# Performance work log

Hardware: AMD Instinct MI355X
Metric: run time of the kernel (lower is better)

Reference implementation:

```python
import jax, jax.numpy as jnp
import numpy as np

B = 1024          # number of graphs (subjects)
N1_PER = 116      # nodes per graph, branch 1 (AAL atlas)
N2_PER = 200      # nodes per graph, branch 2 (CC200 atlas)
DEG = 16          # sparsified adjacency degree
H = 32            # hidden_dim
NUM_CLASSES = 2


def _make_graph(key, b, n, deg):
    """Block-diagonal sparse adjacency in COO form, deg edges per node within its block."""
    N = b * n
    E = N * deg
    rows = jnp.repeat(jnp.arange(N, dtype=jnp.int32), deg)
    offs = jax.random.randint(jax.random.fold_in(key, 0), (E,), 0, n, dtype=jnp.int32)
    cols = (rows // n) * n + offs
    vals = jax.random.uniform(jax.random.fold_in(key, 1), (E,), dtype=jnp.float32)
    return rows, cols, vals


def setup_inputs() -> dict:
    key = jax.random.key(0)
    ks = jax.random.split(key, 20)
    rows1, cols1, vals1 = _make_graph(ks[0], B, N1_PER, DEG)
    rows2, cols2, vals2 = _make_graph(ks[1], B, N2_PER, DEG)
    x1 = jax.random.normal(ks[2], (B * N1_PER, N1_PER), dtype=jnp.float32)
    x2 = jax.random.normal(ks[3], (B * N2_PER, N2_PER), dtype=jnp.float32)
    s = 0.1
    inp = {
        "rows1": rows1, "cols1": cols1, "vals1": vals1, "x1": x1,
        "rows2": rows2, "cols2": cols2, "vals2": vals2, "x2": x2,
        # GCN branch 116
        "W1a": jax.random.normal(ks[4], (N1_PER, H), dtype=jnp.float32) * s,
        "b1a": jnp.zeros((H,), jnp.float32),
        "W1b": jax.random.normal(ks[5], (H, H), dtype=jnp.float32) * s,
        "b1b": jnp.zeros((H,), jnp.float32),
        # GCN branch 200
        "W2a": jax.random.normal(ks[6], (N2_PER, H), dtype=jnp.float32) * s,
        "b2a": jnp.zeros((H,), jnp.float32),
        "W2b": jax.random.normal(ks[7], (H, H), dtype=jnp.float32) * s,
        "b2b": jnp.zeros((H,), jnp.float32),
        # MLP head (stored as (in, out))
        "fc1_W": jax.random.normal(ks[8], (4 * H, H), dtype=jnp.float32) * s,
        "fc1_b": jnp.zeros((H,), jnp.float32),
        "fc2_W": jax.random.normal(ks[9], (H, H // 2), dtype=jnp.float32) * s,
        "fc2_b": jnp.zeros((H // 2,), jnp.float32),
        "fc3_W": jax.random.normal(ks[10], (H // 2, NUM_CLASSES), dtype=jnp.float32) * s,
        "fc3_b": jnp.zeros((NUM_CLASSES,), jnp.float32),
    }
    return inp


def _gcn(rows, cols, vals, x, W, b):
    # support = X @ W  (dense GEMM), then sparse aggregation A @ support, then bias
    support = x @ W                              # [N, H]
    msg = vals[:, None] * support[cols]          # gather + scale, [E, H]
    agg = jax.ops.segment_sum(msg, rows, num_segments=x.shape[0])  # scatter-add
    return agg + b


def _branch(rows, cols, vals, x, Wa, ba, Wb, bb, n_per):
    h = jax.nn.relu(_gcn(rows, cols, vals, x, Wa, ba))
    h = jax.nn.relu(_gcn(rows, cols, vals, h, Wb, bb))
    h = h.reshape(-1, n_per, h.shape[-1])        # [B, n, H]
    return jnp.concatenate([h.mean(axis=1), h.max(axis=1)], axis=1)  # [B, 2H]


def reference(rows1, cols1, vals1, x1, rows2, cols2, vals2, x2,
              W1a, b1a, W1b, b1b, W2a, b2a, W2b, b2b,
              fc1_W, fc1_b, fc2_W, fc2_b, fc3_W, fc3_b):
    f116 = _branch(rows1, cols1, vals1, x1, W1a, b1a, W1b, b1b, N1_PER)
    f200 = _branch(rows2, cols2, vals2, x2, W2a, b2a, W2b, b2b, N2_PER)
    x = jnp.concatenate([f116, f200], axis=1)    # [B, 4H]
    h = jax.nn.relu(x @ fc1_W + fc1_b)           # dropout is identity at inference
    h = jax.nn.relu(h @ fc2_W + fc2_b)
    logits = h @ fc3_W + fc3_b                   # [B, 2]
    return logits
```

## Files before the change

### kernel.cpp

```cpp
#include <hip/hip_runtime.h>

#define NB 1024
#define N1P 116
#define N2P 200
#define HD 32


template <int ST>
__device__ __forceinline__ void agg_phase(int base, int NPv,
                                          const int* __restrict__ cols,
                                          const float* __restrict__ vals,
                                          const float* __restrict__ sup,
                                          float bias, float* __restrict__ outh,
                                          int tid) {
    const int h = tid & 31;
    for (int n = tid >> 5; n < NPv; n += 8) {
        const int4* c4 = (const int4*)(cols + ((size_t)base + n) * 16);
        const float4* v4 = (const float4*)(vals + ((size_t)base + n) * 16);
        float a = bias;
#pragma unroll
        for (int q = 0; q < 4; ++q) {
            const int4 c = c4[q];
            const float4 v = v4[q];
            a += v.x * sup[(c.x - base) * ST + h];
            a += v.y * sup[(c.y - base) * ST + h];
            a += v.z * sup[(c.z - base) * ST + h];
            a += v.w * sup[(c.w - base) * ST + h];
        }
        outh[n * ST + h] = fmaxf(a, 0.f);
    }
}

template <int NP>
__device__ void branch_graph(int g,
                             const float* __restrict__ X,
                             const int* __restrict__ cols,
                             const float* __restrict__ vals,
                             const float* __restrict__ Wa,
                             const float* __restrict__ ba,
                             const float* __restrict__ Wb,
                             const float* __restrict__ bb,
                             float* __restrict__ feats, int foff,
                             float* sSup, float* sH) {
    constexpr int ST = 33;
    constexpr int KC = 16;
    constexpr int SXS = 20;
    constexpr int NSLOT = NP * 4;
    constexpr int PSL = (NSLOT + 255) / 256;

    const int tid = threadIdx.x;
    const int base = g * NP;
    const float* xg = X + (size_t)base * NP;
    const float bA = ba[tid & 31];
    const float bB = bb[tid & 31];

    float* sX = sSup;

    float acc[32];
#pragma unroll
    for (int c = 0; c < 32; ++c) acc[c] = 0.f;

    const int NC = (NP + KC - 1) / KC;

    float4 cur[PSL], nxt[PSL];

    auto load_chunk = [&](int kc, float4* buf) {
        const int k0 = kc * KC;
        const int kw = (NP - k0) < KC ? (NP - k0) : KC;
        const int pieces = kw >> 2;
#pragma unroll
        for (int q = 0; q < PSL; ++q) {
            const int i = tid + q * 256;
            float4 v = make_float4(0.f, 0.f, 0.f, 0.f);
            if (i < NSLOT) {
                const int row = i >> 2, p = i & 3;
                if (p < pieces)
                    v = *(const float4*)(xg + (size_t)row * NP + k0 + p * 4);
            }
            buf[q] = v;
        }
    };
    auto store_chunk = [&](const float4* buf) {
#pragma unroll
        for (int q = 0; q < PSL; ++q) {
            const int i = tid + q * 256;
            if (i < NSLOT) {
                const int row = i >> 2, p = i & 3;
                *(float4*)&sX[row * SXS + p * 4] = buf[q];
            }
        }
    };

    load_chunk(0, cur);
#pragma unroll 1
    for (int kc = 0; kc < NC; ++kc) {
        __syncthreads();
        store_chunk(cur);
        __syncthreads();
        if (kc + 1 < NC) load_chunk(kc + 1, nxt);
        const int k0 = kc * KC;
        const int kw = (NP - k0) < KC ? (NP - k0) : KC;
        if (tid < NP) {
            const float* xrow = &sX[tid * SXS];
            const float* wb0 = Wa + (size_t)k0 * 32;
#pragma unroll 1
            for (int k4 = 0; k4 < kw; k4 += 4) {
                const float4 x4 = *(const float4*)&xrow[k4];
#pragma unroll
                for (int kk = 0; kk < 4; ++kk) {
                    const float xs = (&x4.x)[kk];
                    const float* w = wb0 + (k4 + kk) * 32;
#pragma unroll
                    for (int c4 = 0; c4 < 8; ++c4) {
                        const float4 wv = *(const float4*)&w[c4 * 4];
                        acc[c4 * 4 + 0] += xs * wv.x;
                        acc[c4 * 4 + 1] += xs * wv.y;
                        acc[c4 * 4 + 2] += xs * wv.z;
                        acc[c4 * 4 + 3] += xs * wv.w;
                    }
                }
            }
        }
#pragma unroll
        for (int q = 0; q < PSL; ++q) cur[q] = nxt[q];
    }
    __syncthreads();

    if (tid < NP) {
#pragma unroll
        for (int c4 = 0; c4 < 8; ++c4) {
            float4 o;
            o.x = acc[c4 * 4 + 0]; o.y = acc[c4 * 4 + 1];
            o.z = acc[c4 * 4 + 2]; o.w = acc[c4 * 4 + 3];
            *(float4*)&sSup[tid * ST + c4 * 4] = o;
        }
    }
    __syncthreads();

    agg_phase<ST>(base, NP, cols, vals, sSup, bA, sH, tid);
    __syncthreads();

    if (tid < NP) {
        float acc2[32];
#pragma unroll
        for (int c = 0; c < 32; ++c) acc2[c] = 0.f;
        const float* xrow = &sH[tid * ST];
#pragma unroll 1
        for (int k4 = 0; k4 < 32; k4 += 4) {
            const float4 x4 = *(const float4*)&xrow[k4];
#pragma unroll
            for (int kk = 0; kk < 4; ++kk) {
                const float xs = (&x4.x)[kk];
                const float* w = Wb + (k4 + kk) * 32;
#pragma unroll
                for (int c4 = 0; c4 < 8; ++c4) {
                    const float4 wv = *(const float4*)&w[c4 * 4];
                    acc2[c4 * 4 + 0] += xs * wv.x;
                    acc2[c4 * 4 + 1] += xs * wv.y;
                    acc2[c4 * 4 + 2] += xs * wv.z;
                    acc2[c4 * 4 + 3] += xs * wv.w;
                }
            }
        }
#pragma unroll
        for (int c4 = 0; c4 < 8; ++c4) {
            float4 o;
            o.x = acc2[c4 * 4 + 0]; o.y = acc2[c4 * 4 + 1];
            o.z = acc2[c4 * 4 + 2]; o.w = acc2[c4 * 4 + 3];
            *(float4*)&sSup[tid * ST + c4 * 4] = o;
        }
    }
    __syncthreads();

    agg_phase<ST>(base, NP, cols, vals, sSup, bB, sH, tid);
    __syncthreads();

    const int h = tid & 31, sl = tid >> 5;
    float sum = 0.f, mx = -1e30f;
    for (int n = sl; n < NP; n += 8) {
        const float v = sH[n * ST + h];
        sum += v;
        mx = fmaxf(mx, v);
    }
    float* sS = sSup;
    float* sM = sSup + 256;
    sS[tid] = sum;
    sM[tid] = mx;
    __syncthreads();
    if (tid < 32) {
#pragma unroll
        for (int q = 1; q < 8; ++q) {
            sum += sS[tid + 32 * q];
            mx = fmaxf(mx, sM[tid + 32 * q]);
        }
        feats[(size_t)g * 128 + foff + tid] = sum * (1.0f / NP);
        feats[(size_t)g * 128 + foff + 32 + tid] = mx;
    }
}

__global__ __launch_bounds__(256, 3) void fused_branches(
        const float* __restrict__ x1, const int* __restrict__ cols1,
        const float* __restrict__ vals1,
        const float* __restrict__ W1a, const float* __restrict__ b1a,
        const float* __restrict__ W1b, const float* __restrict__ b1b,
        const float* __restrict__ x2, const int* __restrict__ cols2,
        const float* __restrict__ vals2,
        const float* __restrict__ W2a, const float* __restrict__ b2a,
        const float* __restrict__ W2b, const float* __restrict__ b2b,
        float* __restrict__ feats) {
    __shared__ float sSup[N2P * 33];
    __shared__ float sH[N2P * 33];
    const int bid = blockIdx.x;
    if (bid < NB) {
        branch_graph<N1P>(bid, x1, cols1, vals1, W1a, b1a, W1b, b1b, feats, 0,
                          sSup, sH);
    } else {
        branch_graph<N2P>(bid - NB, x2, cols2, vals2, W2a, b2a, W2b, b2b, feats,
                          64, sSup, sH);
    }
}

__global__ __launch_bounds__(256) void mlp_head(const float* __restrict__ feats,
                                                const float* __restrict__ W1,
                                                const float* __restrict__ b1,
                                                const float* __restrict__ W2,
                                                const float* __restrict__ b2,
                                                const float* __restrict__ W3,
                                                const float* __restrict__ b3,
                                                float* __restrict__ out) {
    __shared__ float sW1[128 * 32];
    __shared__ float sW2[32 * 16];
    __shared__ float sW3[16 * 2];
    __shared__ float sB1[32], sB2[16], sB3[2];
    __shared__ float sF[8 * 128];
    __shared__ float sH1[8 * 32];
    __shared__ float sH2[8 * 16];

    const int tid = threadIdx.x;
    for (int idx = tid; idx < 128 * 32; idx += 256) sW1[idx] = W1[idx];
    for (int idx = tid; idx < 32 * 16; idx += 256) sW2[idx] = W2[idx];
    if (tid < 32) { sW3[tid] = W3[tid]; sB1[tid] = b1[tid]; }
    if (tid < 16) sB2[tid] = b2[tid];
    if (tid < 2) sB3[tid] = b3[tid];
    const long g0 = (long)blockIdx.x * 8;
    for (int idx = tid; idx < 1024; idx += 256) sF[idx] = feats[g0 * 128 + idx];
    __syncthreads();

    const int g = tid >> 5, h = tid & 31;
    float a1 = sB1[h];
#pragma unroll 4
    for (int k = 0; k < 128; ++k) a1 += sF[g * 128 + k] * sW1[k * 32 + h];
    sH1[g * 32 + h] = fmaxf(a1, 0.f);
    __syncthreads();

    if (h < 16) {
        float a2 = sB2[h];
#pragma unroll
        for (int k = 0; k < 32; ++k) a2 += sH1[g * 32 + k] * sW2[k * 16 + h];
        sH2[g * 16 + h] = fmaxf(a2, 0.f);
    }
    __syncthreads();

    if (h < 2) {
        float a3 = sB3[h];
#pragma unroll
        for (int k = 0; k < 16; ++k) a3 += sH2[g * 16 + k] * sW3[k * 2 + h];
        out[(g0 + g) * 2 + h] = a3;
    }
}

extern "C" void kernel_launch(void* const* d_in, const int* in_sizes, int n_in,
                              void* d_out, int out_size, void* d_ws, size_t ws_size,
                              hipStream_t stream) {
    const int*   cols1 = (const int*)d_in[1];
    const float* vals1 = (const float*)d_in[2];
    const float* x1    = (const float*)d_in[3];
    const int*   cols2 = (const int*)d_in[5];
    const float* vals2 = (const float*)d_in[6];
    const float* x2    = (const float*)d_in[7];
    const float* W1a = (const float*)d_in[8];
    const float* b1a = (const float*)d_in[9];
    const float* W1b = (const float*)d_in[10];
    const float* b1b = (const float*)d_in[11];
    const float* W2a = (const float*)d_in[12];
    const float* b2a = (const float*)d_in[13];
    const float* W2b = (const float*)d_in[14];
    const float* b2b = (const float*)d_in[15];
    const float* fc1_W = (const float*)d_in[16];
    const float* fc1_b = (const float*)d_in[17];
    const float* fc2_W = (const float*)d_in[18];
    const float* fc2_b = (const float*)d_in[19];
    const float* fc3_W = (const float*)d_in[20];
    const float* fc3_b = (const float*)d_in[21];
    float* out = (float*)d_out;

    float* feats = (float*)d_ws;

    fused_branches<<<2 * NB, 256, 0, stream>>>(
        x1, cols1, vals1, W1a, b1a, W1b, b1b,
        x2, cols2, vals2, W2a, b2a, W2b, b2b, feats);

    mlp_head<<<NB / 8, 256, 0, stream>>>(feats, fc1_W, fc1_b, fc2_W, fc2_b,
                                         fc3_W, fc3_b, out);
}
```

Baseline: 492.4 us.

## Split first-layer GEMM into a separate row-tiled kernel before per-graph aggregation

The first GCN matmul (X@Wa) moves out of the per-graph fused kernel into its own kernel. That kernel tiles 256 rows per block with double-buffered shared-memory chunks and writes the support matrices to workspace. A second kernel per graph loads the precomputed support, runs both aggregations, the second small GEMM and the pooling. The aim is to decouple the bandwidth-heavy GEMM from the graph-size-limited block structure and raise occupancy, at the cost of an extra global round trip for the support matrices (about 40 MB). The old fused path is kept as a fallback when the workspace is too small.

```diff
diff --git a/kernel.cpp b/kernel.cpp
--- a/kernel.cpp
+++ b/kernel.cpp
@@ -4,6 +4,8 @@
 #define N1P 116
 #define N2P 200
 #define HD 32
+#define T1 464
+#define T2 800
 
 
 template <int ST>
@@ -29,6 +31,203 @@
         }
         outh[n * ST + h] = fmaxf(a, 0.f);
     }
+}
+
+template <int K>
+__device__ void gemm1_tile(const float* __restrict__ xg,
+                           const float* __restrict__ W,
+                           float* __restrict__ Sout, float* sX) {
+    constexpr int KC = 16;
+    constexpr int SXS = 20;
+    constexpr int NC = (K + KC - 1) / KC;
+    const int tid = threadIdx.x;
+
+    float acc[32];
+#pragma unroll
+    for (int c = 0; c < 32; ++c) acc[c] = 0.f;
+
+    float4 cur[4];
+    auto load_chunk = [&](int kc) {
+        const int k0 = kc * KC;
+        const int kw = (K - k0) < KC ? (K - k0) : KC;
+        const int pieces = kw >> 2;
+#pragma unroll
+        for (int q = 0; q < 4; ++q) {
+            const int i = tid + q * 256;
+            const int row = i >> 2, p = i & 3;
+            float4 v = make_float4(0.f, 0.f, 0.f, 0.f);
+            if (p < pieces)
+                v = *(const float4*)(xg + (size_t)row * K + k0 + p * 4);
+            cur[q] = v;
+        }
+    };
+
+    load_chunk(0);
+#pragma unroll 1
+    for (int kc = 0; kc < NC; ++kc) {
+        float* sb = sX + (kc & 1) * (256 * SXS);
+#pragma unroll
+        for (int q = 0; q < 4; ++q) {
+            const int i = tid + q * 256;
+            *(float4*)&sb[(i >> 2) * SXS + (i & 3) * 4] = cur[q];
+        }
+        __syncthreads();
+        if (kc + 1 < NC) load_chunk(kc + 1);
+        const int k0 = kc * KC;
+        const int kw = (K - k0) < KC ? (K - k0) : KC;
+        const float* xrow = &sb[tid * SXS];
+        const float* wb0 = W + (size_t)k0 * 32;
+#pragma unroll 1
+        for (int k4 = 0; k4 < kw; k4 += 4) {
+            const float4 x4 = *(const float4*)&xrow[k4];
+#pragma unroll
+            for (int kk = 0; kk < 4; ++kk) {
+                const float xs = (&x4.x)[kk];
+                const float* w = wb0 + (k4 + kk) * 32;
+#pragma unroll
+                for (int c4 = 0; c4 < 8; ++c4) {
+                    const float4 wv = *(const float4*)&w[c4 * 4];
+                    acc[c4 * 4 + 0] += xs * wv.x;
+                    acc[c4 * 4 + 1] += xs * wv.y;
+                    acc[c4 * 4 + 2] += xs * wv.z;
+                    acc[c4 * 4 + 3] += xs * wv.w;
+                }
+            }
+        }
+    }
+
+    float* srow = Sout + (size_t)tid * 32;
+#pragma unroll
+    for (int c4 = 0; c4 < 8; ++c4) {
+        float4 o;
+        o.x = acc[c4 * 4 + 0]; o.y = acc[c4 * 4 + 1];
+        o.z = acc[c4 * 4 + 2]; o.w = acc[c4 * 4 + 3];
+        *(float4*)&srow[c4 * 4] = o;
+    }
+}
+
+__global__ __launch_bounds__(256, 4) void gemm1_kernel(
+        const float* __restrict__ x1, const float* __restrict__ W1a,
+        float* __restrict__ S1,
+        const float* __restrict__ x2, const float* __restrict__ W2a,
+        float* __restrict__ S2) {
+    __shared__ float sX[2 * 256 * 20];
+    const int bid = blockIdx.x;
+    if (bid < T1) {
+        gemm1_tile<N1P>(x1 + (size_t)bid * 256 * N1P, W1a,
+                        S1 + (size_t)bid * 256 * 32, sX);
+    } else {
+        const int t = bid - T1;
+        gemm1_tile<N2P>(x2 + (size_t)t * 256 * N2P, W2a,
+                        S2 + (size_t)t * 256 * 32, sX);
+    }
+}
+
+template <int NP>
+__device__ void graph_phase(int g, const float* __restrict__ S,
+                            const int* __restrict__ cols,
+                            const float* __restrict__ vals,
+                            const float* __restrict__ ba,
+                            const float* __restrict__ Wb,
+                            const float* __restrict__ bb,
+                            float* __restrict__ feats, int foff,
+                            float* sSup, float* sH) {
+    constexpr int ST = 33;
+    const int tid = threadIdx.x;
+    const int base = g * NP;
+    const float bA = ba[tid & 31];
+    const float bB = bb[tid & 31];
+
+    const float* Sg = S + (size_t)base * 32;
+    constexpr int PIECES = NP * 8;
+    constexpr int PSL = (PIECES + 255) / 256;
+#pragma unroll
+    for (int q = 0; q < PSL; ++q) {
+        const int i = tid + q * 256;
+        if (i < PIECES) {
+            const float4 v = *(const float4*)(Sg + (size_t)i * 4);
+            *(float4*)&sSup[(i >> 3) * ST + (i & 7) * 4] = v;
+        }
+    }
+    __syncthreads();
+
+    agg_phase<ST>(base, NP, cols, vals, sSup, bA, sH, tid);
+    __syncthreads();
+
+    if (tid < NP) {
+        float acc2[32];
+#pragma unroll
+        for (int c = 0; c < 32; ++c) acc2[c] = 0.f;
+        const float* xrow = &sH[tid * ST];
+#pragma unroll 1
+        for (int k4 = 0; k4 < 32; k4 += 4) {
+            const float4 x4 = *(const float4*)&xrow[k4];
+#pragma unroll
+            for (int kk = 0; kk < 4; ++kk) {
+                const float xs = (&x4.x)[kk];
+                const float* w = Wb + (k4 + kk) * 32;
+#pragma unroll
+                for (int c4 = 0; c4 < 8; ++c4) {
+                    const float4 wv = *(const float4*)&w[c4 * 4];
+                    acc2[c4 * 4 + 0] += xs * wv.x;
+                    acc2[c4 * 4 + 1] += xs * wv.y;
+                    acc2[c4 * 4 + 2] += xs * wv.z;
+                    acc2[c4 * 4 + 3] += xs * wv.w;
+                }
+            }
+        }
+#pragma unroll
+        for (int c4 = 0; c4 < 8; ++c4) {
+            float4 o;
+            o.x = acc2[c4 * 4 + 0]; o.y = acc2[c4 * 4 + 1];
+            o.z = acc2[c4 * 4 + 2]; o.w = acc2[c4 * 4 + 3];
+            *(float4*)&sSup[tid * ST + c4 * 4] = o;
+        }
+    }
+    __syncthreads();
+
+    agg_phase<ST>(base, NP, cols, vals, sSup, bB, sH, tid);
+    __syncthreads();
+
+    const int h = tid & 31, sl = tid >> 5;
+    float sum = 0.f, mx = -1e30f;
+    for (int n = sl; n < NP; n += 8) {
+        const float v = sH[n * ST + h];
+        sum += v;
+        mx = fmaxf(mx, v);
+    }
+    float* sS = sSup;
+    float* sM = sSup + 256;
+    sS[tid] = sum;
+    sM[tid] = mx;
+    __syncthreads();
+    if (tid < 32) {
+#pragma unroll
+        for (int q = 1; q < 8; ++q) {
+            sum += sS[tid + 32 * q];
+            mx = fmaxf(mx, sM[tid + 32 * q]);
+        }
+        feats[(size_t)g * 128 + foff + tid] = sum * (1.0f / NP);
+        feats[(size_t)g * 128 + foff + 32 + tid] = mx;
+    }
+}
+
+__global__ __launch_bounds__(256, 3) void graph_fused(
+        const float* __restrict__ S1, const int* __restrict__ cols1,
+        const float* __restrict__ vals1, const float* __restrict__ b1a,
+        const float* __restrict__ W1b, const float* __restrict__ b1b,
+        const float* __restrict__ S2, const int* __restrict__ cols2,
+        const float* __restrict__ vals2, const float* __restrict__ b2a,
+        const float* __restrict__ W2b, const float* __restrict__ b2b,
+        float* __restrict__ feats) {
+    __shared__ float sSup[N2P * 33];
+    __shared__ float sH[N2P * 33];
+    const int bid = blockIdx.x;
+    const int g = bid >> 1;
+    if ((bid & 1) == 0)
+        graph_phase<N1P>(g, S1, cols1, vals1, b1a, W1b, b1b, feats, 0, sSup, sH);
+    else
+        graph_phase<N2P>(g, S2, cols2, vals2, b2a, W2b, b2b, feats, 64, sSup, sH);
 }
 
 template <int NP>
@@ -295,10 +494,23 @@
     float* out = (float*)d_out;
 
     float* feats = (float*)d_ws;
-
-    fused_branches<<<2 * NB, 256, 0, stream>>>(
-        x1, cols1, vals1, W1a, b1a, W1b, b1b,
-        x2, cols2, vals2, W2a, b2a, W2b, b2b, feats);
+    const size_t FEATS_N = (size_t)NB * 128;
+    const size_t S1_N = (size_t)NB * N1P * 32;
+    const size_t S2_N = (size_t)NB * N2P * 32;
+    const size_t need = (FEATS_N + S1_N + S2_N) * sizeof(float);
+
+    if (ws_size >= need) {
+        float* S1 = feats + FEATS_N;
+        float* S2 = S1 + S1_N;
+        gemm1_kernel<<<T1 + T2, 256, 0, stream>>>(x1, W1a, S1, x2, W2a, S2);
+        graph_fused<<<2 * NB, 256, 0, stream>>>(
+            S1, cols1, vals1, b1a, W1b, b1b,
+            S2, cols2, vals2, b2a, W2b, b2b, feats);
+    } else {
+        fused_branches<<<2 * NB, 256, 0, stream>>>(
+            x1, cols1, vals1, W1a, b1a, W1b, b1b,
+            x2, cols2, vals2, W2a, b2a, W2b, b2b, feats);
+    }
 
     mlp_head<<<NB / 8, 256, 0, stream>>>(feats, fc1_W, fc1_b, fc2_W, fc2_b,
                                          fc3_W, fc3_b, out);
```

New measurement: 495.3 us. No clear change (+0.6%).
